# Kernel optimization log

Hardware: AMD Instinct MI355X
Metric: run time of the kernel (lower is better)

Reference implementation:

```python
import jax, jax.numpy as jnp
import numpy as np

N = 100000      # nodes
E = 1600000     # edges (avg degree 16)
IN_F, HID, OUT_F, NC = 384, 128, 64, 2
EPS = 1e-5
NEG_SLOPE = 0.01


def _layernorm(x, g, b):
    m = jnp.mean(x, axis=-1, keepdims=True)
    v = jnp.var(x, axis=-1, keepdims=True)
    return (x - m) * jax.lax.rsqrt(v + EPS) * g + b


def _graph_conv(x, edge_index, edge_weight, w_rel, b_rel, w_root):
    # PyG GraphConv: lin_rel(scatter_add(w_e * x[src] -> dst)) + lin_root(x)
    src, dst = edge_index[0], edge_index[1]
    msg = x[src] * edge_weight[:, None]                      # [E, C]
    agg = jax.ops.segment_sum(msg, dst, num_segments=x.shape[0])  # [N, C]
    return agg @ w_rel.T + b_rel + x @ w_root.T


def _xavier(key, shape):
    fan_in, fan_out = shape[1], shape[0]
    lim = float(np.sqrt(6.0 / (fan_in + fan_out)))
    return jax.random.uniform(key, shape, jnp.float32, -lim, lim)


def setup_inputs() -> dict:
    key = jax.random.key(0)
    ks = jax.random.split(key, 10)
    x = jax.random.normal(ks[0], (N, IN_F), jnp.float32)
    edge_index = jax.random.randint(ks[1], (2, E), 0, N, jnp.int64)
    edge_attr = jax.random.uniform(ks[2], (E,), jnp.float32)
    return {
        "x": x,
        "edge_index": edge_index,
        "edge_attr": edge_attr,
        "ln1_g": jnp.ones((IN_F,), jnp.float32),
        "ln1_b": jnp.zeros((IN_F,), jnp.float32),
        "fc1_w": _xavier(ks[3], (HID, IN_F)),
        "fc1_b": jnp.zeros((HID,), jnp.float32),
        "c1_wrel": _xavier(ks[4], (HID, HID)),
        "c1_brel": jnp.zeros((HID,), jnp.float32),
        "c1_wroot": _xavier(ks[5], (HID, HID)),
        "c2_wrel": _xavier(ks[6], (OUT_F, HID)),
        "c2_brel": jnp.zeros((OUT_F,), jnp.float32),
        "c2_wroot": _xavier(ks[7], (OUT_F, HID)),
        "ln2_g": jnp.ones((OUT_F,), jnp.float32),
        "ln2_b": jnp.zeros((OUT_F,), jnp.float32),
        "fc2_w": _xavier(ks[8], (NC, OUT_F)),
        "fc2_b": jnp.zeros((NC,), jnp.float32),
    }


def reference(x, edge_index, edge_attr,
              ln1_g, ln1_b, fc1_w, fc1_b,
              c1_wrel, c1_brel, c1_wroot,
              c2_wrel, c2_brel, c2_wroot,
              ln2_g, ln2_b, fc2_w, fc2_b):
    h = _layernorm(x, ln1_g, ln1_b) @ fc1_w.T + fc1_b          # [N, HID]
    h = _graph_conv(h, edge_index, edge_attr, c1_wrel, c1_brel, c1_wroot)
    h = jax.nn.leaky_relu(h, NEG_SLOPE)
    h = _graph_conv(h, edge_index, edge_attr, c2_wrel, c2_brel, c2_wroot)
    h = jax.nn.leaky_relu(h, NEG_SLOPE)                        # [N, OUT_F]
    out = _layernorm(h, ln2_g, ln2_b) @ fc2_w.T + fc2_b        # [N, NC]
    return out
```

## Files before the change

### kernel.cpp

```cpp
#include <hip/hip_runtime.h>
#include <hip/hip_bf16.h>

#define N_IN_F 384
#define N_HID  128
#define N_OUT  64

typedef unsigned short ushort_t;
typedef __attribute__((ext_vector_type(8))) short short8v;
typedef __attribute__((ext_vector_type(4))) float floatx4;

union U8 { uint4 v; unsigned short u[8]; };

__device__ __forceinline__ float bfu2f(unsigned short s){
    union { unsigned i; float f; } c; c.i = ((unsigned)s) << 16; return c.f;
}
__device__ __forceinline__ unsigned short f2bfu(float f){
    __hip_bfloat16 h = __float2bfloat16(f);
    union { __hip_bfloat16 h; unsigned short u; } c; c.h = h; return c.u;
}

__device__ __forceinline__ float loadS(const void* p, size_t i, int fm){
    return fm ? bfu2f(((const unsigned short*)p)[i]) : ((const float*)p)[i];
}

__global__ void k_detect_all(const int* __restrict__ ei, const unsigned* __restrict__ xw,
                             int* __restrict__ modep){
    int lane = threadIdx.x & 63;
    int zi = 0;
    if (lane < 32) zi = ei[2*lane + 1];
    int cnt = 0;
    #pragma unroll
    for (int q = 0; q < 8; q++){
        unsigned w = xw[lane*8 + q];
        unsigned elo = (w >> 7) & 0xff;
        cnt += (elo >= 118 && elo <= 134) ? 1 : 0;
    }
    #pragma unroll
    for (int m = 32; m; m >>= 1){ zi |= __shfl_xor(zi, m, 64); cnt += __shfl_xor(cnt, m, 64); }
    if (lane == 0 && blockIdx.x == 0){
        modep[0] = (zi == 0) ? 1 : 0;
        modep[1] = (cnt >= 256) ? 1 : 0;
    }
}

__device__ __forceinline__ int edge_src(const int* ei, int e, int i, int mode){
    return mode ? ei[2*(size_t)i] : ei[i];
}
__device__ __forceinline__ int edge_dst(const int* ei, int e, int i, int mode){
    return mode ? ei[2*(size_t)e + 2*(size_t)i] : ei[(size_t)e + i];
}

__global__ void k_hist(const int* __restrict__ ei, int e, int n, const int* __restrict__ modep,
                       int* __restrict__ deg){
    int i = blockIdx.x * 256 + threadIdx.x;
    if (i >= e) return;
    int mode = modep[0];
    int d = edge_dst(ei, e, i, mode);
    if ((unsigned)d >= (unsigned)n) return;
    atomicAdd(&deg[d], 1);
}

__global__ __launch_bounds__(1024) void k_blksum(
    const int* __restrict__ deg, int n, int* __restrict__ part)
{
    __shared__ int s[1024];
    int i = blockIdx.x * 1024 + threadIdx.x;
    s[threadIdx.x] = (i < n) ? deg[i] : 0;
    __syncthreads();
    for (int off = 512; off; off >>= 1){
        if (threadIdx.x < off) s[threadIdx.x] += s[threadIdx.x + off];
        __syncthreads();
    }
    if (threadIdx.x == 0) part[blockIdx.x] = s[0];
}

__global__ __launch_bounds__(128) void k_scanpart(
    int* __restrict__ part, int nb, int* __restrict__ rowoff, int n)
{
    __shared__ int s[128];
    int t = threadIdx.x;
    if (nb <= 128){
        int v = (t < nb) ? part[t] : 0;
        s[t] = v; __syncthreads();
        #pragma unroll
        for (int off = 1; off < 128; off <<= 1){
            int tmp = (t >= off) ? s[t - off] : 0;
            __syncthreads();
            s[t] += tmp;
            __syncthreads();
        }
        if (t < nb) part[t] = s[t] - v;
        if (t == 127) rowoff[n] = s[127];
    } else if (t == 0){
        int run = 0;
        for (int b = 0; b < nb; b++){ int tt = part[b]; part[b] = run; run += tt; }
        rowoff[n] = run;
    }
}

__global__ __launch_bounds__(1024) void k_scanblk(
    int* __restrict__ deg, const int* __restrict__ part, int n, int* __restrict__ rowoff)
{
    __shared__ int s[1024];
    int t = threadIdx.x;
    int i = blockIdx.x * 1024 + t;
    int v = (i < n) ? deg[i] : 0;
    s[t] = v; __syncthreads();
    for (int off = 1; off < 1024; off <<= 1){
        int tmp = (t >= off) ? s[t - off] : 0;
        __syncthreads();
        s[t] += tmp;
        __syncthreads();
    }
    if (i < n){
        int excl = s[t] - v + part[blockIdx.x];
        rowoff[i] = excl;
        deg[i]    = excl;
    }
}

__global__ void k_scatter(const int* __restrict__ ei, const void* __restrict__ ea,
                          int e, int n, const int* __restrict__ modep,
                          int* __restrict__ cursor, int2* __restrict__ colw)
{
    int i = blockIdx.x * 256 + threadIdx.x;
    if (i >= e) return;
    int mode = modep[0], fm = modep[1];
    int d = edge_dst(ei, e, i, mode);
    if ((unsigned)d >= (unsigned)n) return;
    int s = edge_src(ei, e, i, mode);
    if ((unsigned)s >= (unsigned)n) s = 0;
    int pos = atomicAdd(&cursor[d], 1);
    if ((unsigned)pos >= (unsigned)e) return;
    int2 pk; pk.x = s; pk.y = __float_as_int(loadS(ea, i, fm));
    colw[pos] = pk;
}

__global__ __launch_bounds__(64) void k_prep_w1(
    const void* __restrict__ W, const void* __restrict__ g, const void* __restrict__ b,
    const void* __restrict__ fc1b, const int* __restrict__ fmp,
    ushort_t* __restrict__ Wp, float* __restrict__ u, float* __restrict__ v)
{
    int fm = fmp[0];
    int j = blockIdx.x, lane = threadIdx.x;
    float su = 0.f, sv = 0.f;
    for (int k = lane; k < N_IN_F; k += 64){
        float w  = loadS(W, (size_t)j*N_IN_F + k, fm);
        float gk = loadS(g, k, fm);
        float bk = loadS(b, k, fm);
        unsigned short pw = f2bfu(gk * w);
        Wp[(size_t)j*N_IN_F + k] = pw;
        su += bfu2f(pw);
        sv += bk * w;
    }
    #pragma unroll
    for (int m = 32; m; m >>= 1){ su += __shfl_xor(su, m, 64); sv += __shfl_xor(sv, m, 64); }
    if (lane == 0){
        u[j] = su;
        v[j] = sv + loadS(fc1b, j, fm);
    }
}

__global__ void k_cvt4(const void* __restrict__ p0, const void* __restrict__ p1,
                       const void* __restrict__ p2, const void* __restrict__ p3,
                       const int* __restrict__ fmp, ushort_t* __restrict__ o)
{
    int fm = fmp[0];
    int i = blockIdx.x * 256 + threadIdx.x;
    if (i >= 49152) return;
    const void* p; int off;
    if (i < 16384)      { p = p0; off = i; }
    else if (i < 32768) { p = p1; off = i - 16384; }
    else if (i < 40960) { p = p2; off = i - 32768; }
    else                { p = p3; off = i - 40960; }
    o[i] = f2bfu(loadS(p, off, fm));
}

__global__ __launch_bounds__(256) void k_gemm1_mfma(
    const void* __restrict__ x, const int* __restrict__ fmp,
    const ushort_t* __restrict__ Wp,
    const float* __restrict__ u, const float* __restrict__ v,
    ushort_t* __restrict__ out, int n)
{
    __shared__ ushort_t As[128*40];
    __shared__ ushort_t Bs[128*40];
    int fm = fmp[0];
    int t = threadIdx.x;
    int wave = t >> 6, lane = t & 63;
    int r16 = lane & 15, kq = lane >> 4;
    int m0 = blockIdx.x * 128;
    int mw = m0 + wave * 32;

    int sq = t & 3, srow = t >> 2;
    int bcol = t & 127, bhalf = t >> 7;

    floatx4 acc[2][8];
    #pragma unroll
    for (int a = 0; a < 2; a++)
        #pragma unroll
        for (int c = 0; c < 8; c++) acc[a][c] = (floatx4){0.f,0.f,0.f,0.f};
    float s1[2] = {0.f,0.f}, s2[2] = {0.f,0.f};

    for (int ks = 0; ks < 12; ks++){
        int kb = ks*32;
        #pragma unroll
        for (int pass = 0; pass < 2; pass++){
            int row  = srow + pass*64;
            int grow = min(m0 + row, n - 1);
            union { ushort_t u[8]; uint4 v4; } w;
            if (fm){
                w.v4 = *(const uint4*)((const ushort_t*)x + (size_t)grow*N_IN_F + kb + sq*8);
            } else {
                const float* xf = (const float*)x + (size_t)grow*N_IN_F + kb + sq*8;
                floatx4 p = *(const floatx4*)xf;
                floatx4 q4 = *(const floatx4*)(xf + 4);
                w.u[0]=f2bfu(p[0]); w.u[1]=f2bfu(p[1]); w.u[2]=f2bfu(p[2]); w.u[3]=f2bfu(p[3]);
                w.u[4]=f2bfu(q4[0]); w.u[5]=f2bfu(q4[1]); w.u[6]=f2bfu(q4[2]); w.u[7]=f2bfu(q4[3]);
            }
            *(uint4*)(As + row*40 + sq*8) = w.v4;
        }
        {
            const ushort_t* wp = Wp + (size_t)bcol*N_IN_F + kb + bhalf*16;
            uint4 b0 = *(const uint4*)wp;
            uint4 b1 = *(const uint4*)(wp + 8);
            *(uint4*)(Bs + bcol*40 + bhalf*16)     = b0;
            *(uint4*)(Bs + bcol*40 + bhalf*16 + 8) = b1;
        }
        __syncthreads();
        short8v af[2], bfr[8];
        #pragma unroll
        for (int mi = 0; mi < 2; mi++)
            af[mi] = *(const short8v*)(As + (wave*32 + mi*16 + r16)*40 + kq*8);
        #pragma unroll
        for (int ni = 0; ni < 8; ni++)
            bfr[ni] = *(const short8v*)(Bs + (ni*16 + r16)*40 + kq*8);
        #pragma unroll
        for (int mi = 0; mi < 2; mi++){
            #pragma unroll
            for (int q = 0; q < 8; q++){
                float f = bfu2f((unsigned short)af[mi][q]);
                s1[mi] += f; s2[mi] += f*f;
            }
            #pragma unroll
            for (int ni = 0; ni < 8; ni++)
                acc[mi][ni] = __builtin_amdgcn_mfma_f32_16x16x32_bf16(af[mi], bfr[ni], acc[mi][ni], 0, 0, 0);
        }
        __syncthreads();
    }

    float mu[2], rs[2];
    #pragma unroll
    for (int mi = 0; mi < 2; mi++){
        s1[mi] += __shfl_xor(s1[mi], 16, 64); s1[mi] += __shfl_xor(s1[mi], 32, 64);
        s2[mi] += __shfl_xor(s2[mi], 16, 64); s2[mi] += __shfl_xor(s2[mi], 32, 64);
        mu[mi] = s1[mi] * (1.f/384.f);
        float var = fmaxf(s2[mi] * (1.f/384.f) - mu[mi]*mu[mi], 0.f);
        rs[mi] = rsqrtf(var + 1e-5f);
    }

    #pragma unroll
    for (int mi = 0; mi < 2; mi++){
        int ib = mw + mi*16 + kq*4;
        float mm[4], rr[4];
        #pragma unroll
        for (int r = 0; r < 4; r++){
            mm[r] = __shfl(mu[mi], kq*4 + r, 64);
            rr[r] = __shfl(rs[mi], kq*4 + r, 64);
        }
        #pragma unroll
        for (int ni = 0; ni < 8; ni++){
            int j = ni*16 + r16;
            float uj = u[j], vj = v[j];
            #pragma unroll
            for (int r = 0; r < 4; r++){
                int ii = ib + r;
                float val = rr[r]*acc[mi][ni][r] - rr[r]*mm[r]*uj + vj;
                if (ii < n) out[(size_t)ii*N_HID + j] = f2bfu(val);
            }
        }
    }
}

__global__ __launch_bounds__(256) void k_conv1_mfma(
    const ushort_t* __restrict__ A1, const ushort_t* __restrict__ A2,
    const ushort_t* __restrict__ W1, const ushort_t* __restrict__ W2,
    const void* __restrict__ bias, const int* __restrict__ fmp,
    ushort_t* __restrict__ out, int n)
{
    __shared__ ushort_t As[128*40];
    __shared__ ushort_t Bs[128*40];
    int fm = fmp[0];
    int t = threadIdx.x;
    int wave = t >> 6, lane = t & 63;
    int r16 = lane & 15, kq = lane >> 4;
    int m0 = blockIdx.x * 128;
    int mw = m0 + wave * 32;

    int sq = t & 3, srow = t >> 2;
    int bcol = t & 127, bhalf = t >> 7;

    floatx4 acc[2][8];
    #pragma unroll
    for (int a = 0; a < 2; a++)
        #pragma unroll
        for (int c = 0; c < 8; c++) acc[a][c] = (floatx4){0.f,0.f,0.f,0.f};

    #pragma unroll
    for (int ks = 0; ks < 8; ks++){
        const ushort_t* Asrc = (ks < 4) ? A1 : A2;
        const ushort_t* Wsrc = (ks < 4) ? W1 : W2;
        int kb = (ks & 3)*32;
        #pragma unroll
        for (int pass = 0; pass < 2; pass++){
            int row  = srow + pass*64;
            int grow = min(m0 + row, n - 1);
            uint4 w = *(const uint4*)(Asrc + (size_t)grow*N_HID + kb + sq*8);
            *(uint4*)(As + row*40 + sq*8) = w;
        }
        {
            const ushort_t* wp = Wsrc + (size_t)bcol*N_HID + kb + bhalf*16;
            uint4 b0 = *(const uint4*)wp;
            uint4 b1 = *(const uint4*)(wp + 8);
            *(uint4*)(Bs + bcol*40 + bhalf*16)     = b0;
            *(uint4*)(Bs + bcol*40 + bhalf*16 + 8) = b1;
        }
        __syncthreads();
        short8v af[2], bfr[8];
        #pragma unroll
        for (int mi = 0; mi < 2; mi++)
            af[mi] = *(const short8v*)(As + (wave*32 + mi*16 + r16)*40 + kq*8);
        #pragma unroll
        for (int ni = 0; ni < 8; ni++)
            bfr[ni] = *(const short8v*)(Bs + (ni*16 + r16)*40 + kq*8);
        #pragma unroll
        for (int mi = 0; mi < 2; mi++)
            #pragma unroll
            for (int ni = 0; ni < 8; ni++)
                acc[mi][ni] = __builtin_amdgcn_mfma_f32_16x16x32_bf16(af[mi], bfr[ni], acc[mi][ni], 0, 0, 0);
        __syncthreads();
    }

    #pragma unroll
    for (int mi = 0; mi < 2; mi++){
        int ib = mw + mi*16 + kq*4;
        #pragma unroll
        for (int ni = 0; ni < 8; ni++){
            int j = ni*16 + r16;
            float bb = loadS(bias, j, fm);
            #pragma unroll
            for (int r = 0; r < 4; r++){
                int ii = ib + r;
                float val = acc[mi][ni][r] + bb;
                val = (val >= 0.f) ? val : 0.01f * val;
                if (ii < n) out[(size_t)ii*N_HID + j] = f2bfu(val);
            }
        }
    }
}

__global__ __launch_bounds__(256) void k_conv2_final(
    const ushort_t* __restrict__ A1, const ushort_t* __restrict__ A2,
    const ushort_t* __restrict__ W1, const ushort_t* __restrict__ W2,
    const void* __restrict__ bias,
    const void* __restrict__ gam, const void* __restrict__ bet,
    const void* __restrict__ Wfc, const void* __restrict__ bfc,
    const int* __restrict__ fmp, void* __restrict__ out, int n)
{
    __shared__ ushort_t As[128*40];
    __shared__ ushort_t Bs[64*40];
    int fm = fmp[0];
    int t = threadIdx.x;
    int wave = t >> 6, lane = t & 63;
    int r16 = lane & 15, kq = lane >> 4;
    int m0 = blockIdx.x * 128;
    int mw = m0 + wave * 32;

    int sq = t & 3, srow = t >> 2;
    int bcol = t & 63, bseg = t >> 6;

    floatx4 acc[2][4];
    #pragma unroll
    for (int a = 0; a < 2; a++)
        #pragma unroll
        for (int c = 0; c < 4; c++) acc[a][c] = (floatx4){0.f,0.f,0.f,0.f};

    #pragma unroll
    for (int ks = 0; ks < 8; ks++){
        const ushort_t* Asrc = (ks < 4) ? A1 : A2;
        const ushort_t* Wsrc = (ks < 4) ? W1 : W2;
        int kb = (ks & 3)*32;
        #pragma unroll
        for (int pass = 0; pass < 2; pass++){
            int row  = srow + pass*64;
            int grow = min(m0 + row, n - 1);
            uint4 w = *(const uint4*)(Asrc + (size_t)grow*N_HID + kb + sq*8);
            *(uint4*)(As + row*40 + sq*8) = w;
        }
        {
            uint4 b0 = *(const uint4*)(Wsrc + (size_t)bcol*N_HID + kb + bseg*8);
            *(uint4*)(Bs + bcol*40 + bseg*8) = b0;
        }
        __syncthreads();
        short8v af[2], bfr[4];
        #pragma unroll
        for (int mi = 0; mi < 2; mi++)
            af[mi] = *(const short8v*)(As + (wave*32 + mi*16 + r16)*40 + kq*8);
        #pragma unroll
        for (int ni = 0; ni < 4; ni++)
            bfr[ni] = *(const short8v*)(Bs + (ni*16 + r16)*40 + kq*8);
        #pragma unroll
        for (int mi = 0; mi < 2; mi++)
            #pragma unroll
            for (int ni = 0; ni < 4; ni++)
                acc[mi][ni] = __builtin_amdgcn_mfma_f32_16x16x32_bf16(af[mi], bfr[ni], acc[mi][ni], 0, 0, 0);
        __syncthreads();
    }

    float b0 = loadS(bfc, 0, fm), b1 = loadS(bfc, 1, fm);
    #pragma unroll
    for (int mi = 0; mi < 2; mi++){
        float s[4] = {}, s2[4] = {};
        #pragma unroll
        for (int ni = 0; ni < 4; ni++){
            int j = ni*16 + r16;
            float bb = loadS(bias, j, fm);
            #pragma unroll
            for (int r = 0; r < 4; r++){
                float val = acc[mi][ni][r] + bb;
                val = (val >= 0.f) ? val : 0.01f * val;
                acc[mi][ni][r] = val;
                s[r] += val; s2[r] += val*val;
            }
        }
        #pragma unroll
        for (int m = 1; m < 16; m <<= 1){
            #pragma unroll
            for (int r = 0; r < 4; r++){
                s[r]  += __shfl_xor(s[r],  m, 64);
                s2[r] += __shfl_xor(s2[r], m, 64);
            }
        }
        float mu[4], rstd[4];
        #pragma unroll
        for (int r = 0; r < 4; r++){
            mu[r] = s[r] * (1.f/64.f);
            float var = fmaxf(s2[r] * (1.f/64.f) - mu[r]*mu[r], 0.f);
            rstd[r] = rsqrtf(var + 1e-5f);
        }
        float p0[4] = {}, p1[4] = {};
        #pragma unroll
        for (int ni = 0; ni < 4; ni++){
            int j = ni*16 + r16;
            float gj = loadS(gam, j, fm), bj = loadS(bet, j, fm);
            float w0 = loadS(Wfc, j, fm), w1 = loadS(Wfc, 64 + j, fm);
            #pragma unroll
            for (int r = 0; r < 4; r++){
                float zn = (acc[mi][ni][r] - mu[r]) * rstd[r] * gj + bj;
                p0[r] += zn * w0;
                p1[r] += zn * w1;
            }
        }
        #pragma unroll
        for (int m = 1; m < 16; m <<= 1){
            #pragma unroll
            for (int r = 0; r < 4; r++){
                p0[r] += __shfl_xor(p0[r], m, 64);
                p1[r] += __shfl_xor(p1[r], m, 64);
            }
        }
        if (r16 == 0){
            #pragma unroll
            for (int r = 0; r < 4; r++){
                int ii = mw + mi*16 + kq*4 + r;
                if (ii >= n) continue;
                float o0 = p0[r] + b0, o1 = p1[r] + b1;
                if (fm){
                    unsigned pk = ((unsigned)f2bfu(o1) << 16) | (unsigned)f2bfu(o0);
                    *(unsigned*)((ushort_t*)out + (size_t)ii*2) = pk;
                } else {
                    float2 f2; f2.x = o0; f2.y = o1;
                    *(float2*)((float*)out + (size_t)ii*2) = f2;
                }
            }
        }
    }
}

__global__ __launch_bounds__(256) void k_agg(
    const int* __restrict__ rowoff, const int2* __restrict__ colw,
    const ushort_t* __restrict__ src_mat,
    ushort_t* __restrict__ out, int n, int eTot)
{
    int t = threadIdx.x;
    int lane = t & 63;
    int d = blockIdx.x * 4 + (t >> 6);
    if (d >= n) return;
    int grp = lane >> 4;
    int c16 = lane & 15;
    int e0 = rowoff[d], e1 = rowoff[d+1];
    e0 = max(0, min(e0, eTot));
    e1 = max(e0, min(e1, eTot));
    float acc[8] = {};
    for (int e = e0 + grp; e < e1; e += 4){
        int2 cw = colw[e];
        int s = cw.x;
        if ((unsigned)s >= (unsigned)n) s = 0;
        float wv = __int_as_float(cw.y);
        U8 u; u.v = *(const uint4*)(src_mat + (size_t)s*N_HID + c16*8);
        #pragma unroll
        for (int q = 0; q < 8; q++) acc[q] += wv * bfu2f(u.u[q]);
    }
    #pragma unroll
    for (int q = 0; q < 8; q++){
        acc[q] += __shfl_xor(acc[q], 16, 64);
        acc[q] += __shfl_xor(acc[q], 32, 64);
    }
    if (grp == 0){
        union { ushort_t u[8]; uint4 v; } P;
        #pragma unroll
        for (int q = 0; q < 8; q++) P.u[q] = f2bfu(acc[q]);
        *(uint4*)(out + (size_t)d*N_HID + c16*8) = P.v;
    }
}

extern "C" void kernel_launch(void* const* d_in, const int* in_sizes, int n_in,
                              void* d_out, int out_size, void* d_ws, size_t ws_size,
                              hipStream_t stream)
{
    const void* x     = d_in[0];
    const int*  ei    = (const int*)d_in[1];
    const void* ea    = d_in[2];
    const void* ln1g  = d_in[3];
    const void* ln1b  = d_in[4];
    const void* fc1w  = d_in[5];
    const void* fc1b  = d_in[6];
    const void* c1rel = d_in[7];
    const void* c1bre = d_in[8];
    const void* c1roo = d_in[9];
    const void* c2rel = d_in[10];
    const void* c2bre = d_in[11];
    const void* c2roo = d_in[12];
    const void* ln2g  = d_in[13];
    const void* ln2b  = d_in[14];
    const void* fc2w  = d_in[15];
    const void* fc2b  = d_in[16];
    (void)n_in; (void)out_size; (void)ws_size;

    const int n = in_sizes[0] / N_IN_F;
    const int e = in_sizes[2];

    char* wsp = (char*)d_ws;
    size_t off = 0;
    auto alloc = [&](size_t bytes) -> char* {
        char* p = wsp + off; off += (bytes + 255) & ~(size_t)255; return p;
    };
    int*      deg    = (int*)  alloc((size_t)n * 4);
    int*      rowoff = (int*)  alloc((size_t)(n+1) * 4);
    int*      part   = (int*)  alloc(4096);
    int*      modep  = (int*)  alloc(256);
    int2*     colw   = (int2*) alloc((size_t)e * 8);
    float*    u      = (float*)alloc(128 * 4);
    float*    v      = (float*)alloc(128 * 4);
    ushort_t* Wp     = (ushort_t*)alloc((size_t)N_HID * N_IN_F * 2);
    ushort_t* cw     = (ushort_t*)alloc((size_t)49152 * 2);
    ushort_t* h1     = (ushort_t*)alloc((size_t)n * N_HID * 2);
    ushort_t* agg1   = (ushort_t*)alloc((size_t)n * N_HID * 2);
    ushort_t* g1     = (ushort_t*)alloc((size_t)n * N_HID * 2);
    ushort_t* agg2   = h1;

    hipMemsetAsync(deg, 0, (size_t)n * 4, stream);
    k_detect_all<<<1, 64, 0, stream>>>(ei, (const unsigned*)x, modep);

    int nb = (n + 1023) / 1024;
    k_hist    <<<(e + 255) / 256, 256, 0, stream>>>(ei, e, n, modep, deg);
    k_blksum  <<<nb, 1024, 0, stream>>>(deg, n, part);
    k_scanpart<<<1, 128, 0, stream>>>(part, nb, rowoff, n);
    k_scanblk <<<nb, 1024, 0, stream>>>(deg, part, n, rowoff);
    k_scatter <<<(e + 255) / 256, 256, 0, stream>>>(ei, ea, e, n, modep, deg, colw);

    k_prep_w1<<<N_HID, 64, 0, stream>>>(fc1w, ln1g, ln1b, fc1b, modep + 1, Wp, u, v);
    k_cvt4   <<<(49152 + 255) / 256, 256, 0, stream>>>(c1rel, c1roo, c2rel, c2roo, modep + 1, cw);

    k_gemm1_mfma<<<(n + 127) / 128, 256, 0, stream>>>(x, modep + 1, Wp, u, v, h1, n);

    k_agg<<<(n + 3) / 4, 256, 0, stream>>>(rowoff, colw, h1, agg1, n, e);
    k_conv1_mfma<<<(n + 127) / 128, 256, 0, stream>>>(agg1, h1, cw, cw + 16384, c1bre, modep + 1, g1, n);

    k_agg<<<(n + 3) / 4, 256, 0, stream>>>(rowoff, colw, g1, agg2, n, e);
    k_conv2_final<<<(n + 127) / 128, 256, 0, stream>>>(agg2, g1, cw + 32768, cw + 40960, c2bre,
                                                       ln2g, ln2b, fc2w, fc2b, modep + 1, d_out, n);
}
```

Baseline: 670.2 us.

## Replace atomic CSR scatter with two-pass bucketed coarse/fine scatter

The histogram kernel now records each edge's rank within its destination row, so final CSR positions are known without a second pass of atomics. A coarse kernel partitions each 2048-edge chunk into 8192-position buckets in shared memory and writes them out contiguously. A fine kernel per bucket then writes the entries into colw, keeping the scattered writes within a small address window. This aims to replace random global atomics and scattered writes with more local traffic, but adds an extra 16-byte-per-edge temporary pass and two extra launches.

```diff
diff --git a/kernel.cpp b/kernel.cpp
--- a/kernel.cpp
+++ b/kernel.cpp
@@ -51,13 +51,13 @@
 }
 
 __global__ void k_hist(const int* __restrict__ ei, int e, int n, const int* __restrict__ modep,
-                       int* __restrict__ deg){
+                       int* __restrict__ deg, unsigned* __restrict__ rel){
     int i = blockIdx.x * 256 + threadIdx.x;
     if (i >= e) return;
     int mode = modep[0];
     int d = edge_dst(ei, e, i, mode);
     if ((unsigned)d >= (unsigned)n) return;
-    atomicAdd(&deg[d], 1);
+    rel[i] = (unsigned)atomicAdd(&deg[d], 1);
 }
 
 __global__ __launch_bounds__(1024) void k_blksum(
@@ -134,6 +134,97 @@
     if ((unsigned)pos >= (unsigned)e) return;
     int2 pk; pk.x = s; pk.y = __float_as_int(loadS(ea, i, fm));
     colw[pos] = pk;
+}
+
+#define SC_CHUNK 2048
+#define SC_BSHIFT 13
+#define SC_MAXB 1024
+__global__ __launch_bounds__(256) void k_scoarse(
+    const int* __restrict__ ei, const void* __restrict__ ea,
+    const unsigned* __restrict__ rel, const int* __restrict__ rowoff,
+    const int* __restrict__ modep, int e, int n, int B,
+    int4* __restrict__ tmp, int* __restrict__ off2)
+{
+    __shared__ int  hcnt[SC_MAXB];
+    __shared__ int  hoff[SC_MAXB + 1];
+    __shared__ int4 stage[SC_CHUNK];
+    int t = threadIdx.x;
+    int c = blockIdx.x;
+    int chunk0 = c * SC_CHUNK;
+    int mode = modep[0], fm = modep[1];
+
+    for (int q = t; q < B; q += 256) hcnt[q] = 0;
+    __syncthreads();
+
+    int  pos[8], sv[8], wv[8];
+    bool val[8];
+    #pragma unroll
+    for (int k = 0; k < 8; k++){
+        int i = chunk0 + k*256 + t;
+        val[k] = false;
+        if (i < e){
+            int d = edge_dst(ei, e, i, mode);
+            if ((unsigned)d < (unsigned)n){
+                int s = edge_src(ei, e, i, mode);
+                if ((unsigned)s >= (unsigned)n) s = 0;
+                int p = rowoff[d] + (int)rel[i];
+                pos[k] = p; sv[k] = s; wv[k] = __float_as_int(loadS(ea, i, fm));
+                val[k] = true;
+                atomicAdd(&hcnt[p >> SC_BSHIFT], 1);
+            }
+        }
+    }
+    __syncthreads();
+    if (t == 0){
+        int run = 0;
+        for (int q = 0; q < B; q++){ hoff[q] = run; run += hcnt[q]; }
+        hoff[B] = run;
+    }
+    __syncthreads();
+    for (int q = t; q < B; q += 256) hcnt[q] = 0;
+    for (int q = t; q <= B; q += 256) off2[(size_t)c*(B+1) + q] = hoff[q];
+    __syncthreads();
+    #pragma unroll
+    for (int k = 0; k < 8; k++){
+        if (val[k]){
+            int b = pos[k] >> SC_BSHIFT;
+            int slot = hoff[b] + atomicAdd(&hcnt[b], 1);
+            stage[slot] = make_int4(pos[k], sv[k], wv[k], 0);
+        }
+    }
+    __syncthreads();
+    int tot = hoff[B];
+    for (int idx = t; idx < tot; idx += 256)
+        tmp[(size_t)chunk0 + idx] = stage[idx];
+}
+
+__global__ __launch_bounds__(512) void k_sfine(
+    const int4* __restrict__ tmp, const int* __restrict__ off2,
+    int B, int nchunks, int2* __restrict__ colw)
+{
+    int b = blockIdx.x;
+    int wv = threadIdx.x >> 6, lane = threadIdx.x & 63;
+    const int NW = 8;
+    int c = wv;
+    if (c >= nchunks) return;
+    int s0 = off2[(size_t)c*(B+1) + b];
+    int s1 = off2[(size_t)c*(B+1) + b + 1];
+    while (true){
+        int cn = c + NW;
+        int n0 = 0, n1 = 0;
+        if (cn < nchunks){
+            n0 = off2[(size_t)cn*(B+1) + b];
+            n1 = off2[(size_t)cn*(B+1) + b + 1];
+        }
+        int len = s1 - s0;
+        size_t base = (size_t)c * SC_CHUNK + s0;
+        for (int k = lane; k < len; k += 64){
+            int4 ent = tmp[base + k];
+            colw[ent.x] = make_int2(ent.y, ent.z);
+        }
+        if (cn >= nchunks) break;
+        c = cn; s0 = n0; s1 = n1;
+    }
 }
 
 __global__ __launch_bounds__(64) void k_prep_w1(
@@ -549,6 +640,9 @@
     const int n = in_sizes[0] / N_IN_F;
     const int e = in_sizes[2];
 
+    const int nchunks = (e + SC_CHUNK - 1) / SC_CHUNK;
+    const int B = (e + (1 << SC_BSHIFT) - 1) >> SC_BSHIFT;
+
     char* wsp = (char*)d_ws;
     size_t off = 0;
     auto alloc = [&](size_t bytes) -> char* {
@@ -559,6 +653,9 @@
     int*      part   = (int*)  alloc(4096);
     int*      modep  = (int*)  alloc(256);
     int2*     colw   = (int2*) alloc((size_t)e * 8);
+    unsigned* rel    = (unsigned*)alloc((size_t)e * 4);
+    int4*     stmp   = (int4*) alloc((size_t)e * 16);
+    int*      off2   = (int*)  alloc((size_t)nchunks * (B+1) * 4);
     float*    u      = (float*)alloc(128 * 4);
     float*    v      = (float*)alloc(128 * 4);
     ushort_t* Wp     = (ushort_t*)alloc((size_t)N_HID * N_IN_F * 2);
@@ -572,11 +669,17 @@
     k_detect_all<<<1, 64, 0, stream>>>(ei, (const unsigned*)x, modep);
 
     int nb = (n + 1023) / 1024;
-    k_hist    <<<(e + 255) / 256, 256, 0, stream>>>(ei, e, n, modep, deg);
+    k_hist    <<<(e + 255) / 256, 256, 0, stream>>>(ei, e, n, modep, deg, rel);
     k_blksum  <<<nb, 1024, 0, stream>>>(deg, n, part);
     k_scanpart<<<1, 128, 0, stream>>>(part, nb, rowoff, n);
     k_scanblk <<<nb, 1024, 0, stream>>>(deg, part, n, rowoff);
-    k_scatter <<<(e + 255) / 256, 256, 0, stream>>>(ei, ea, e, n, modep, deg, colw);
+
+    if (B <= SC_MAXB){
+        k_scoarse<<<nchunks, 256, 0, stream>>>(ei, ea, rel, rowoff, modep, e, n, B, stmp, off2);
+        k_sfine  <<<B, 512, 0, stream>>>(stmp, off2, B, nchunks, colw);
+    } else {
+        k_scatter<<<(e + 255) / 256, 256, 0, stream>>>(ei, ea, e, n, modep, deg, colw);
+    }
 
     k_prep_w1<<<N_HID, 64, 0, stream>>>(fc1w, ln1g, ln1b, fc1b, modep + 1, Wp, u, v);
     k_cvt4   <<<(49152 + 255) / 256, 256, 0, stream>>>(c1rel, c1roo, c2rel, c2roo, modep + 1, cw);
```

After: 658.7 us. No clear change (-1.7%).
